# Kernel tuning notes

Hardware: AMD Instinct MI355X
Metric: run time of the kernel (lower is better)

The kernel has to match this reference:

```python
import jax, jax.numpy as jnp
import numpy as np

N, E = 100000, 800000
H, C = 4, 32
HC = H * C


def setup_inputs() -> dict:
    key = jax.random.key(0)
    ks = jax.random.split(key, 32)

    def lin(k, fi, fo):
        return jax.random.normal(k, (fi, fo), jnp.float32) / np.sqrt(fi)

    inp = {
        "x": jax.random.normal(ks[0], (N, 2), jnp.float32),
        "edge_index": jax.random.randint(ks[1], (2, E), 0, N, jnp.int64),
        "edge_attr": jax.random.normal(ks[2], (E, 1), jnp.float32),
        # layer 0 (in=2)
        "Wq0": lin(ks[3], 2, HC), "bq0": jnp.zeros((HC,), jnp.float32),
        "Wk0": lin(ks[4], 2, HC), "bk0": jnp.zeros((HC,), jnp.float32),
        "Wv0": lin(ks[5], 2, HC), "bv0": jnp.zeros((HC,), jnp.float32),
        "We0": lin(ks[6], 1, HC),
        "Ws0": lin(ks[7], 2, HC), "bs0": jnp.zeros((HC,), jnp.float32),
        # layer 1 (in=HC)
        "Wq1": lin(ks[8], HC, HC), "bq1": jnp.zeros((HC,), jnp.float32),
        "Wk1": lin(ks[9], HC, HC), "bk1": jnp.zeros((HC,), jnp.float32),
        "Wv1": lin(ks[10], HC, HC), "bv1": jnp.zeros((HC,), jnp.float32),
        "We1": lin(ks[11], 1, HC),
        "Ws1": lin(ks[12], HC, HC), "bs1": jnp.zeros((HC,), jnp.float32),
        # classifier
        "Wc1": lin(ks[13], HC, 128), "bc1": jnp.zeros((128,), jnp.float32),
        "Wc2": lin(ks[14], 128, 64), "bc2": jnp.zeros((64,), jnp.float32),
        "Wc3": lin(ks[15], 64, 1), "bc3": jnp.zeros((1,), jnp.float32),
    }
    return inp


def _tconv(x, src, dst, edge_attr, Wq, bq, Wk, bk, Wv, bv, We, Ws, bs):
    # PyG TransformerConv (concat=True, root_weight=True, beta=False)
    n = x.shape[0]
    q = (x @ Wq + bq).reshape(n, H, C)
    k = (x @ Wk + bk).reshape(n, H, C)
    v = (x @ Wv + bv).reshape(n, H, C)
    e = (edge_attr @ We).reshape(-1, H, C)            # [E,H,C]
    k_j = k[src] + e
    v_j = v[src] + e
    alpha = jnp.einsum("ehc,ehc->eh", q[dst], k_j) / np.sqrt(C)  # [E,H]
    m = jax.ops.segment_max(alpha, dst, num_segments=n)          # [n,H]
    m = jnp.where(jnp.isfinite(m), m, 0.0)            # nodes with no in-edges
    ex = jnp.exp(alpha - m[dst])
    denom = jax.ops.segment_sum(ex, dst, num_segments=n)
    w = ex / (denom[dst] + 1e-16)                      # per-edge softmax weight
    out = jax.ops.segment_sum(v_j * w[:, :, None], dst, num_segments=n)
    return out.reshape(n, HC) + x @ Ws + bs


def reference(x, edge_index, edge_attr,
              Wq0, bq0, Wk0, bk0, Wv0, bv0, We0, Ws0, bs0,
              Wq1, bq1, Wk1, bk1, Wv1, bv1, We1, Ws1, bs1,
              Wc1, bc1, Wc2, bc2, Wc3, bc3):
    src, dst = edge_index[0], edge_index[1]
    h = jax.nn.relu(_tconv(x, src, dst, edge_attr, Wq0, bq0, Wk0, bk0, Wv0, bv0, We0, Ws0, bs0))
    h = jax.nn.relu(_tconv(h, src, dst, edge_attr, Wq1, bq1, Wk1, bk1, Wv1, bv1, We1, Ws1, bs1))
    # classifier (dropout inactive in eval)
    h = jax.nn.relu(h @ Wc1 + bc1)
    h = jax.nn.relu(h @ Wc2 + bc2)
    return h @ Wc3 + bc3
```

## Files before the change

### kernel.cpp

```cpp
#include <hip/hip_runtime.h>
#include <hip/hip_bf16.h>
#include <cstdio>
#include <cstdint>


typedef short s16x8 __attribute__((ext_vector_type(8)));
typedef float f32x4 __attribute__((ext_vector_type(4)));

static inline int cdiv(int a, int b) { return (a + b - 1) / b; }

#define EXP2F(x) __builtin_amdgcn_exp2f(x)
#define LOG2E 1.4426950408889634f
#define RSC 0.17677669529663687f

__device__ __forceinline__ float bflo(unsigned u) {
    union { unsigned i; float f; } x; x.i = u << 16; return x.f;
}
__device__ __forceinline__ float bfhi(unsigned u) {
    union { unsigned i; float f; } x; x.i = u & 0xffff0000u; return x.f;
}
__device__ __forceinline__ unsigned short f2b(float f) {
    __hip_bfloat16 h = __float2bfloat16(f);
    return *reinterpret_cast<unsigned short*>(&h);
}
__device__ __forceinline__ unsigned packbf(float lo, float hi) {
    return (unsigned)f2b(lo) | ((unsigned)f2b(hi) << 16);
}


__global__ __launch_bounds__(256) void hist_kernel(const int* __restrict__ dst, int E,
                                                   int* __restrict__ counts) {
    int e = blockIdx.x * 256 + threadIdx.x;
    if (e < E) atomicAdd(&counts[dst[e]], 1);
}

__global__ __launch_bounds__(256) void scan_sums(const int* __restrict__ counts, int n,
                                                 int* __restrict__ bsums) {
    __shared__ int red[256];
    int base = blockIdx.x * 2048 + threadIdx.x * 8;
    int s = 0;
#pragma unroll
    for (int j = 0; j < 8; ++j) {
        int i = base + j;
        if (i < n) s += counts[i];
    }
    red[threadIdx.x] = s;
    __syncthreads();
    for (int off = 128; off > 0; off >>= 1) {
        if (threadIdx.x < off) red[threadIdx.x] += red[threadIdx.x + off];
        __syncthreads();
    }
    if (threadIdx.x == 0) bsums[blockIdx.x] = red[0];
}

__global__ void scan_mid(int* bsums, int nb, int* offsets, int n) {
    if (blockIdx.x == 0 && threadIdx.x == 0) {
        int run = 0;
        for (int i = 0; i < nb; ++i) { int t = bsums[i]; bsums[i] = run; run += t; }
        offsets[n] = run;
    }
}

__global__ __launch_bounds__(256) void scan_out(const int* __restrict__ counts, int n,
                                                const int* __restrict__ bsums,
                                                int* __restrict__ offsets) {
    __shared__ int tsum[256];
    int base = blockIdx.x * 2048 + threadIdx.x * 8;
    int v[8];
    int s = 0;
#pragma unroll
    for (int j = 0; j < 8; ++j) {
        int i = base + j;
        v[j] = (i < n) ? counts[i] : 0;
        s += v[j];
    }
    tsum[threadIdx.x] = s;
    __syncthreads();
    for (int off = 1; off < 256; off <<= 1) {
        int x = (threadIdx.x >= (unsigned)off) ? tsum[threadIdx.x - off] : 0;
        __syncthreads();
        tsum[threadIdx.x] += x;
        __syncthreads();
    }
    int excl = tsum[threadIdx.x] - s + bsums[blockIdx.x];
#pragma unroll
    for (int j = 0; j < 8; ++j) {
        int i = base + j;
        if (i < n) { offsets[i] = excl; excl += v[j]; }
    }
}

__global__ __launch_bounds__(256) void scatter_kernel(const int* __restrict__ src,
                                                      const int* __restrict__ dst,
                                                      const float* __restrict__ ea, int E,
                                                      const int* __restrict__ offsets,
                                                      int* __restrict__ counts,
                                                      int* __restrict__ csr_off,
                                                      float* __restrict__ csr_ea) {
    int e = blockIdx.x * 256 + threadIdx.x;
    if (e >= E) return;
    int d = dst[e];
    int r = atomicSub(&counts[d], 1);
    int p = offsets[d] + r - 1;
    csr_off[p] = src[e] << 9;
    csr_ea[p] = ea[e];
}


__global__ __launch_bounds__(256) void pack_w_kernel(
    const float* __restrict__ Wq1, const float* __restrict__ Wk1,
    const float* __restrict__ Wv1, const float* __restrict__ Ws1,
    const float* __restrict__ Wc1, const float* __restrict__ Wc2,
    unsigned short* __restrict__ wpk,
    const float* __restrict__ Wq0, const float* __restrict__ bq0,
    const float* __restrict__ Wk0, const float* __restrict__ bk0,
    const float* __restrict__ We0, float* __restrict__ gcoef) {
    if (blockIdx.x == 352) {
        int t = threadIdx.x;
        if (t < 48) {
            int h = t / 12, r = t % 12, i = r >> 2, j = r & 3;
            const float* A = (i == 0) ? Wq0 : (i == 1) ? (Wq0 + 128) : bq0;
            const float* B = (j == 0) ? Wk0 : (j == 1) ? (Wk0 + 128) : (j == 2) ? We0 : bk0;
            float s = 0.f;
            for (int c = 0; c < 32; ++c) s += A[h * 32 + c] * B[h * 32 + c];
            gcoef[h * 12 + i * 4 + j] = s * (RSC * LOG2E);
        }
        return;
    }
    int idx = blockIdx.x * 256 + threadIdx.x;
    int local, COLS;
    const float* W;
    if (idx < 81920) {
        int m = idx >> 14;
        local = idx & 16383;
        COLS = 128;
        W = (m == 0) ? Wq1 : (m == 1) ? Wk1 : (m == 2) ? Wv1 : (m == 3) ? Ws1 : Wc1;
    } else {
        local = idx - 81920;
        COLS = 64;
        W = Wc2;
    }
    int CT = COLS >> 4;
    int j = local & 7, lane = (local >> 3) & 63, t = local >> 9;
    int ct = t % CT, kc = t / CT;
    int k = kc * 32 + ((lane >> 4) << 3) + j;
    int nn = (ct << 4) + (lane & 15);
    wpk[idx] = f2b(W[k * COLS + nn]);
}


__global__ __launch_bounds__(256) void agg0_kernel(
    const float* __restrict__ x, const float* __restrict__ gcoef,
    float4* __restrict__ agg4,
    const int* __restrict__ offsets, const int* __restrict__ csr_off,
    const float* __restrict__ csr_ea, int n_nodes) {
    int tid = blockIdx.x * 256 + threadIdx.x;
    int n = tid >> 2, h = tid & 3;
    if (n >= n_nodes) return;
    float2 xn = ((const float2*)x)[n];
    const float4* G4 = (const float4*)gcoef;
    float4 g0 = G4[h * 3 + 0], g1 = G4[h * 3 + 1], g2 = G4[h * 3 + 2];
    float c0 = fmaf(xn.y, g1.x, fmaf(xn.x, g0.x, g2.x));
    float c1 = fmaf(xn.y, g1.y, fmaf(xn.x, g0.y, g2.y));
    float c2 = fmaf(xn.y, g1.z, fmaf(xn.x, g0.z, g2.z));
    float c3 = fmaf(xn.y, g1.w, fmaf(xn.x, g0.w, g2.w));
    int beg = offsets[n], end = offsets[n + 1];
    float d = 0.f, X0 = 0.f, X1 = 0.f, EA = 0.f;
    for (int j = beg; j < end; ++j) {
        int off = csr_off[j];
        float e = csr_ea[j];
        float2 xs = *(const float2*)((const char*)x + (off >> 6));
        float al = fmaf(c0, xs.x, fmaf(c1, xs.y, fmaf(c2, e, c3)));
        float w = EXP2F(fminf(al, 72.f));
        d += w;
        X0 = fmaf(w, xs.x, X0);
        X1 = fmaf(w, xs.y, X1);
        EA = fmaf(w, e, EA);
    }
    agg4[(size_t)n * 4 + h] = make_float4(X0, X1, EA, d);
}


__global__ __launch_bounds__(256) void expand0_kernel(
    const float* __restrict__ x, const float4* __restrict__ agg4,
    const float* __restrict__ Wv, const float* __restrict__ bv,
    const float* __restrict__ We, const float* __restrict__ Ws,
    const float* __restrict__ bs, uint2* __restrict__ H0, int n_nodes) {
    int gid = blockIdx.x * 256 + threadIdx.x;
    int n = gid >> 5, g = gid & 31;
    if (n >= n_nodes) return;
    int h = g >> 3;
    float4 ag = agg4[(size_t)n * 4 + h];
    float inv = 1.f / (ag.w + 1e-16f);
    float2 xn = ((const float2*)x)[n];
    float4 wv0 = ((const float4*)Wv)[g], wv1 = ((const float4*)(Wv + 128))[g];
    float4 we = ((const float4*)We)[g], bv4 = ((const float4*)bv)[g];
    float4 ws0 = ((const float4*)Ws)[g], ws1 = ((const float4*)(Ws + 128))[g];
    float4 bs4 = ((const float4*)bs)[g];
    float o0 = fmaf(wv0.x, ag.x, fmaf(wv1.x, ag.y, fmaf(we.x, ag.z, bv4.x * ag.w))) * inv
             + fmaf(xn.x, ws0.x, fmaf(xn.y, ws1.x, bs4.x));
    float o1 = fmaf(wv0.y, ag.x, fmaf(wv1.y, ag.y, fmaf(we.y, ag.z, bv4.y * ag.w))) * inv
             + fmaf(xn.x, ws0.y, fmaf(xn.y, ws1.y, bs4.y));
    float o2 = fmaf(wv0.z, ag.x, fmaf(wv1.z, ag.y, fmaf(we.z, ag.z, bv4.z * ag.w))) * inv
             + fmaf(xn.x, ws0.z, fmaf(xn.y, ws1.z, bs4.z));
    float o3 = fmaf(wv0.w, ag.x, fmaf(wv1.w, ag.y, fmaf(we.w, ag.z, bv4.w * ag.w))) * inv
             + fmaf(xn.x, ws0.w, fmaf(xn.y, ws1.w, bs4.w));
    uint2 o;
    o.x = packbf(fmaxf(o0, 0.f), fmaxf(o1, 0.f));
    o.y = packbf(fmaxf(o2, 0.f), fmaxf(o3, 0.f));
    H0[(size_t)n * 32 + g] = o;
}


__global__ __launch_bounds__(64) void agg1_kernel(
    const uint2* __restrict__ Q2, const unsigned short* __restrict__ KV,
    const float* __restrict__ We, const uint2* __restrict__ S2,
    uint2* __restrict__ Hout, const int* __restrict__ offsets,
    const int* __restrict__ csr_off, const float* __restrict__ csr_ea,
    int n_nodes) {
    int lane = threadIdx.x & 63;
    int h = lane & 31, half = lane >> 5;
    int n = blockIdx.x;
    if (n >= n_nodes) return;
    size_t rb = (size_t)n * 32;
    const float sc = RSC * LOG2E;
    uint2 qp = Q2[rb + h];
    float q0 = bflo(qp.x) * sc, q1 = bfhi(qp.x) * sc;
    float q2 = bflo(qp.y) * sc, q3 = bfhi(qp.y) * sc;
    float4 we4 = ((const float4*)We)[h];
    float qwe = fmaf(q3, we4.w, fmaf(q2, we4.z, fmaf(q1, we4.y, q0 * we4.x)));
    qwe += __shfl_xor(qwe, 1);
    qwe += __shfl_xor(qwe, 2);
    qwe += __shfl_xor(qwe, 4);
    int beg = __builtin_amdgcn_readfirstlane(offsets[n]);
    int end = __builtin_amdgcn_readfirstlane(offsets[n + 1]);
    float dA = 0.f, a0A = 0.f, a1A = 0.f, a2A = 0.f, a3A = 0.f, eA = 0.f;
    float dB = 0.f, a0B = 0.f, a1B = 0.f, a2B = 0.f, a3B = 0.f, eB = 0.f;
    int lane_b = h << 3;
    for (int j = beg + half; j < end; j += 4) {
        int jB = j + 2;
        bool vB = jB < end;
        int jmB = vB ? jB : j;
        int offA = csr_off[j], offB = csr_off[jmB];
        float eaA = csr_ea[j], eaB = csr_ea[jmB];
        const char* kvA = (const char*)KV + (size_t)(unsigned)offA + lane_b;
        const char* kvB = (const char*)KV + (size_t)(unsigned)offB + lane_b;
        uint2 kA = *(const uint2*)kvA;
        uint2 vA = *(const uint2*)(kvA + 256);
        uint2 kB = *(const uint2*)kvB;
        uint2 vB2 = *(const uint2*)(kvB + 256);
        {
            float p = fmaf(q3, bfhi(kA.y), fmaf(q2, bflo(kA.y),
                      fmaf(q1, bfhi(kA.x), q0 * bflo(kA.x))));
            p += __shfl_xor(p, 1);
            p += __shfl_xor(p, 2);
            p += __shfl_xor(p, 4);
            float al = fminf(fmaf(eaA, qwe, p), 72.f);
            float w = EXP2F(al);
            dA += w;
            a0A = fmaf(w, bflo(vA.x), a0A);
            a1A = fmaf(w, bfhi(vA.x), a1A);
            a2A = fmaf(w, bflo(vA.y), a2A);
            a3A = fmaf(w, bfhi(vA.y), a3A);
            eA = fmaf(w, eaA, eA);
        }
        {
            float p = fmaf(q3, bfhi(kB.y), fmaf(q2, bflo(kB.y),
                      fmaf(q1, bfhi(kB.x), q0 * bflo(kB.x))));
            p += __shfl_xor(p, 1);
            p += __shfl_xor(p, 2);
            p += __shfl_xor(p, 4);
            float al = fmaf(eaB, qwe, p);
            al = vB ? al : -3.0e38f;
            float w = EXP2F(fminf(al, 72.f));
            dB += w;
            a0B = fmaf(w, bflo(vB2.x), a0B);
            a1B = fmaf(w, bfhi(vB2.x), a1B);
            a2B = fmaf(w, bflo(vB2.y), a2B);
            a3B = fmaf(w, bfhi(vB2.y), a3B);
            eB = fmaf(w, eaB, eB);
        }
    }
    float d = dA + dB;
    float a0 = a0A + a0B, a1 = a1A + a1B, a2 = a2A + a2B, a3 = a3A + a3B;
    float ea = eA + eB;
    d += __shfl_xor(d, 32);
    a0 += __shfl_xor(a0, 32);
    a1 += __shfl_xor(a1, 32);
    a2 += __shfl_xor(a2, 32);
    a3 += __shfl_xor(a3, 32);
    ea += __shfl_xor(ea, 32);
    if (half == 0) {
        float inv = 1.f / (d + 1e-16f);
        uint2 sp = S2[rb + h];
        uint2 o;
        o.x = packbf(fmaxf(fmaf(a0 + we4.x * ea, inv, bflo(sp.x)), 0.f),
                     fmaxf(fmaf(a1 + we4.y * ea, inv, bfhi(sp.x)), 0.f));
        o.y = packbf(fmaxf(fmaf(a2 + we4.z * ea, inv, bflo(sp.y)), 0.f),
                     fmaxf(fmaf(a3 + we4.w * ea, inv, bfhi(sp.y)), 0.f));
        Hout[rb + h] = o;
    }
}


__global__ __launch_bounds__(256, 2) void gemm4_kernel(
    const unsigned short* __restrict__ Hb, int n_nodes,
    const unsigned short* __restrict__ wpk,
    const float* __restrict__ B0, unsigned short* __restrict__ O0, int ld0,
    const float* __restrict__ B1, unsigned short* __restrict__ O1, int ld1,
    const float* __restrict__ B2, unsigned short* __restrict__ O2, int ld2,
    const float* __restrict__ B3, unsigned short* __restrict__ O3, int ld3) {
    __shared__ unsigned short wbuf[16384];
    __shared__ char tbuf[128 * 272];
    int tid = threadIdx.x;
    int wid = tid >> 6, lane = tid & 63;
    int lr = lane & 15, lk = lane >> 4;
    int nblk = blockIdx.x * 128;

    s16x8 b[2][4];
#pragma unroll
    for (int nt = 0; nt < 2; ++nt) {
        int row = min(nblk + wid * 32 + nt * 16 + lr, n_nodes - 1);
        const s16x8* hp = (const s16x8*)(Hb + (size_t)row * 128);
#pragma unroll
        for (int kc = 0; kc < 4; ++kc) b[nt][kc] = hp[kc * 4 + lk];
    }
    const float* Bm[4] = {B0, B1, B2, B3};
    unsigned short* Om[4] = {O0, O1, O2, O3};
    int ldm[4] = {ld0, ld1, ld2, ld3};

#pragma unroll
    for (int i = 0; i < 8; ++i) {
        int c = i * 256 + tid;
        ((uint4*)wbuf)[c] = ((const uint4*)wpk)[c];
    }
#pragma unroll
    for (int mm = 0; mm < 4; ++mm) {
        __syncthreads();
        f32x4 acc[2][8];
#pragma unroll
        for (int nt = 0; nt < 2; ++nt)
#pragma unroll
            for (int ct = 0; ct < 8; ++ct) acc[nt][ct] = (f32x4){0.f, 0.f, 0.f, 0.f};
#pragma unroll
        for (int kc = 0; kc < 4; ++kc) {
#pragma unroll
            for (int ct = 0; ct < 8; ++ct) {
                s16x8 a = ((const s16x8*)wbuf)[(kc * 8 + ct) * 64 + lane];
                acc[0][ct] = __builtin_amdgcn_mfma_f32_16x16x32_bf16(a, b[0][kc], acc[0][ct], 0, 0, 0);
                acc[1][ct] = __builtin_amdgcn_mfma_f32_16x16x32_bf16(a, b[1][kc], acc[1][ct], 0, 0, 0);
            }
        }
        const float* Bp = Bm[mm];
#pragma unroll
        for (int ct = 0; ct < 8; ++ct) {
            float4 bb = *(const float4*)(Bp + ct * 16 + lk * 4);
#pragma unroll
            for (int nt = 0; nt < 2; ++nt) {
                int rnode = wid * 32 + nt * 16 + lr;
                uint2 o;
                o.x = packbf(acc[nt][ct][0] + bb.x, acc[nt][ct][1] + bb.y);
                o.y = packbf(acc[nt][ct][2] + bb.z, acc[nt][ct][3] + bb.w);
                *(uint2*)(tbuf + rnode * 272 + ct * 32 + lk * 8) = o;
            }
        }
        __syncthreads();
        unsigned short* Op = Om[mm];
        int ld = ldm[mm];
#pragma unroll
        for (int i = 0; i < 8; ++i) {
            int chunk = i * 256 + tid;
            int nd = chunk >> 4, c16 = chunk & 15;
            int ng = nblk + nd;
            uint4 v = *(const uint4*)(tbuf + nd * 272 + c16 * 16);
            if (ng < n_nodes) *(uint4*)(Op + (size_t)ng * ld + c16 * 8) = v;
        }
        if (mm < 3) {
            const uint4* ws = (const uint4*)(wpk + (mm + 1) * 16384);
#pragma unroll
            for (int i = 0; i < 8; ++i) {
                int c = i * 256 + tid;
                ((uint4*)wbuf)[c] = ws[c];
            }
        }
    }
}


__global__ __launch_bounds__(256) void classifier_kernel(
    const unsigned short* __restrict__ H1b, int n_nodes,
    const unsigned short* __restrict__ wc1p, const float* __restrict__ bc1,
    const unsigned short* __restrict__ wc2p, const float* __restrict__ bc2,
    const float* __restrict__ Wc3, const float* __restrict__ bc3,
    float* __restrict__ out) {
    __shared__ char lds_raw[4 * 16 * 272];
    int wid = threadIdx.x >> 6, lane = threadIdx.x & 63;
    int lr = lane & 15, lk = lane >> 4;
    int nb = blockIdx.x * 64 + wid * 16;
    char* tile = lds_raw + wid * 16 * 272;

    s16x8 b[4];
    {
        int row = min(nb + lr, n_nodes - 1);
        const s16x8* hp = (const s16x8*)(H1b + (size_t)row * 128);
#pragma unroll
        for (int kc = 0; kc < 4; ++kc) b[kc] = hp[kc * 4 + lk];
    }
    f32x4 acc[8];
#pragma unroll
    for (int ct = 0; ct < 8; ++ct) acc[ct] = (f32x4){0.f, 0.f, 0.f, 0.f};
#pragma unroll
    for (int kc = 0; kc < 4; ++kc)
#pragma unroll
        for (int ct = 0; ct < 8; ++ct) {
            s16x8 a = ((const s16x8*)wc1p)[(kc * 8 + ct) * 64 + lane];
            acc[ct] = __builtin_amdgcn_mfma_f32_16x16x32_bf16(a, b[kc], acc[ct], 0, 0, 0);
        }
#pragma unroll
    for (int ct = 0; ct < 8; ++ct) {
        float4 bb = *(const float4*)(bc1 + ct * 16 + lk * 4);
        uint2 o;
        o.x = packbf(fmaxf(acc[ct][0] + bb.x, 0.f), fmaxf(acc[ct][1] + bb.y, 0.f));
        o.y = packbf(fmaxf(acc[ct][2] + bb.z, 0.f), fmaxf(acc[ct][3] + bb.w, 0.f));
        *(uint2*)(tile + lr * 272 + ct * 32 + lk * 8) = o;
    }
    __syncthreads();
    s16x8 b2[4];
#pragma unroll
    for (int kc = 0; kc < 4; ++kc)
        b2[kc] = *(const s16x8*)(tile + lr * 272 + kc * 64 + lk * 16);
    f32x4 acc2[4];
#pragma unroll
    for (int ct = 0; ct < 4; ++ct) acc2[ct] = (f32x4){0.f, 0.f, 0.f, 0.f};
#pragma unroll
    for (int kc = 0; kc < 4; ++kc)
#pragma unroll
        for (int ct = 0; ct < 4; ++ct) {
            s16x8 a = ((const s16x8*)wc2p)[(kc * 4 + ct) * 64 + lane];
            acc2[ct] = __builtin_amdgcn_mfma_f32_16x16x32_bf16(a, b2[kc], acc2[ct], 0, 0, 0);
        }
    float part = 0.f;
#pragma unroll
    for (int ct = 0; ct < 4; ++ct) {
        int ch0 = ct * 16 + lk * 4;
        float4 bb = *(const float4*)(bc2 + ch0);
        float4 w3 = *(const float4*)(Wc3 + ch0);
        part += fmaxf(acc2[ct][0] + bb.x, 0.f) * w3.x;
        part += fmaxf(acc2[ct][1] + bb.y, 0.f) * w3.y;
        part += fmaxf(acc2[ct][2] + bb.z, 0.f) * w3.z;
        part += fmaxf(acc2[ct][3] + bb.w, 0.f) * w3.w;
    }
    part += __shfl_xor(part, 16);
    part += __shfl_xor(part, 32);
    if (lk == 0) {
        int node = nb + lr;
        if (node < n_nodes) out[node] = part + bc3[0];
    }
}


extern "C" void kernel_launch(void* const* d_in, const int* in_sizes, int n_in,
                              void* d_out, int out_size, void* d_ws, size_t ws_size,
                              hipStream_t stream) {
    const float* x = (const float*)d_in[0];
    const int* ei = (const int*)d_in[1];
    const float* ea = (const float*)d_in[2];
    const float *Wq0 = (const float*)d_in[3], *bq0 = (const float*)d_in[4];
    const float *Wk0 = (const float*)d_in[5], *bk0 = (const float*)d_in[6];
    const float *Wv0 = (const float*)d_in[7], *bv0 = (const float*)d_in[8];
    const float* We0 = (const float*)d_in[9];
    const float *Ws0 = (const float*)d_in[10], *bs0 = (const float*)d_in[11];
    const float *Wq1 = (const float*)d_in[12], *bq1 = (const float*)d_in[13];
    const float *Wk1 = (const float*)d_in[14], *bk1 = (const float*)d_in[15];
    const float *Wv1 = (const float*)d_in[16], *bv1 = (const float*)d_in[17];
    const float* We1 = (const float*)d_in[18];
    const float *Ws1 = (const float*)d_in[19], *bs1 = (const float*)d_in[20];
    const float *Wc1 = (const float*)d_in[21], *bc1 = (const float*)d_in[22];
    const float *Wc2 = (const float*)d_in[23], *bc2 = (const float*)d_in[24];
    const float *Wc3 = (const float*)d_in[25], *bc3 = (const float*)d_in[26];

    const int N = in_sizes[0] / 2;
    const int E = in_sizes[2];
    const int* src = ei;
    const int* dst = ei + E;

    size_t NM = (size_t)N * 128;
    float4* agg4 = (float4*)d_ws;
    float* gcoef = (float*)(agg4 + (size_t)N * 4);
    unsigned short* H0b = (unsigned short*)(gcoef + 64);
    unsigned short* Qb = H0b + NM;
    unsigned short* KV = Qb + NM;
    unsigned short* S1b = KV + 2 * NM;
    unsigned short* wpk = S1b + NM;
    int* counts = (int*)(wpk + 90112);
    int* offsets = counts + N;
    int* bsums = offsets + N + 1;
    int* csr_off = bsums + 256;
    float* csr_ea = (float*)(csr_off + E);
    size_t need = (size_t)((char*)(csr_ea + E) - (char*)d_ws);
    if (need > ws_size) {
        fprintf(stderr, "kernel_launch: ws too small (need %zu, have %zu)\n", need, ws_size);
        return;
    }

    const int NB_SCAN = cdiv(N, 2048);

    hipMemsetAsync(counts, 0, (size_t)N * 4, stream);
    hist_kernel<<<cdiv(E, 256), 256, 0, stream>>>(dst, E, counts);
    scan_sums<<<NB_SCAN, 256, 0, stream>>>(counts, N, bsums);
    scan_mid<<<1, 64, 0, stream>>>(bsums, NB_SCAN, offsets, N);
    scan_out<<<NB_SCAN, 256, 0, stream>>>(counts, N, bsums, offsets);
    scatter_kernel<<<cdiv(E, 256), 256, 0, stream>>>(src, dst, ea, E, offsets, counts,
                                                     csr_off, csr_ea);
    pack_w_kernel<<<353, 256, 0, stream>>>(Wq1, Wk1, Wv1, Ws1, Wc1, Wc2, wpk,
                                           Wq0, bq0, Wk0, bk0, We0, gcoef);

    agg0_kernel<<<cdiv(N * 4, 256), 256, 0, stream>>>(
        x, gcoef, agg4, offsets, csr_off, csr_ea, N);
    expand0_kernel<<<cdiv(N * 32, 256), 256, 0, stream>>>(
        x, agg4, Wv0, bv0, We0, Ws0, bs0, (uint2*)H0b, N);

    gemm4_kernel<<<cdiv(N, 128), 256, 0, stream>>>(
        H0b, N, wpk,
        bq1, Qb, 128,
        bk1, KV, 256,
        bv1, KV + 128, 256,
        bs1, S1b, 128);
    agg1_kernel<<<N, 64, 0, stream>>>(
        (const uint2*)Qb, KV, We1, (const uint2*)S1b, (uint2*)S1b,
        offsets, csr_off, csr_ea, N);

    classifier_kernel<<<cdiv(N, 64), 256, 0, stream>>>(
        S1b, N, wpk + 65536, bc1, wpk + 81920, bc2, Wc3, bc3, (float*)d_out);
}
```

Before: 353.1 us.

## Interleave CSR offset/attr, widen agg1 to 16-byte loads, stage classifier weights in LDS

Result: slower. 360.3 us (+2.1%).

```diff
diff --git a/kernel.cpp b/kernel.cpp
--- a/kernel.cpp
+++ b/kernel.cpp
@@ -95,15 +95,13 @@
                                                       const float* __restrict__ ea, int E,
                                                       const int* __restrict__ offsets,
                                                       int* __restrict__ counts,
-                                                      int* __restrict__ csr_off,
-                                                      float* __restrict__ csr_ea) {
+                                                      int2* __restrict__ csr) {
     int e = blockIdx.x * 256 + threadIdx.x;
     if (e >= E) return;
     int d = dst[e];
     int r = atomicSub(&counts[d], 1);
     int p = offsets[d] + r - 1;
-    csr_off[p] = src[e] << 9;
-    csr_ea[p] = ea[e];
+    csr[p] = make_int2(src[e] << 9, __float_as_int(ea[e]));
 }
 
 
@@ -152,8 +150,7 @@
 __global__ __launch_bounds__(256) void agg0_kernel(
     const float* __restrict__ x, const float* __restrict__ gcoef,
     float4* __restrict__ agg4,
-    const int* __restrict__ offsets, const int* __restrict__ csr_off,
-    const float* __restrict__ csr_ea, int n_nodes) {
+    const int* __restrict__ offsets, const int2* __restrict__ csr, int n_nodes) {
     int tid = blockIdx.x * 256 + threadIdx.x;
     int n = tid >> 2, h = tid & 3;
     if (n >= n_nodes) return;
@@ -167,9 +164,9 @@
     int beg = offsets[n], end = offsets[n + 1];
     float d = 0.f, X0 = 0.f, X1 = 0.f, EA = 0.f;
     for (int j = beg; j < end; ++j) {
-        int off = csr_off[j];
-        float e = csr_ea[j];
-        float2 xs = *(const float2*)((const char*)x + (off >> 6));
+        int2 ce = csr[j];
+        float e = __int_as_float(ce.y);
+        float2 xs = *(const float2*)((const char*)x + (((unsigned)ce.x) >> 6));
         float al = fmaf(c0, xs.x, fmaf(c1, xs.y, fmaf(c2, e, c3)));
         float w = EXP2F(fminf(al, 72.f));
         d += w;
@@ -213,91 +210,107 @@
 
 
 __global__ __launch_bounds__(64) void agg1_kernel(
-    const uint2* __restrict__ Q2, const unsigned short* __restrict__ KV,
-    const float* __restrict__ We, const uint2* __restrict__ S2,
-    uint2* __restrict__ Hout, const int* __restrict__ offsets,
-    const int* __restrict__ csr_off, const float* __restrict__ csr_ea,
-    int n_nodes) {
+    const uint4* __restrict__ Q4, const unsigned short* __restrict__ KV,
+    const float* __restrict__ We, const uint4* __restrict__ S4,
+    uint4* __restrict__ Hout, const int* __restrict__ offsets,
+    const int2* __restrict__ csr, int n_nodes) {
     int lane = threadIdx.x & 63;
-    int h = lane & 31, half = lane >> 5;
+    int h = lane & 15, g = lane >> 4;
     int n = blockIdx.x;
     if (n >= n_nodes) return;
-    size_t rb = (size_t)n * 32;
+    size_t rb = (size_t)n * 16;
     const float sc = RSC * LOG2E;
-    uint2 qp = Q2[rb + h];
+    uint4 qp = Q4[rb + h];
     float q0 = bflo(qp.x) * sc, q1 = bfhi(qp.x) * sc;
     float q2 = bflo(qp.y) * sc, q3 = bfhi(qp.y) * sc;
-    float4 we4 = ((const float4*)We)[h];
-    float qwe = fmaf(q3, we4.w, fmaf(q2, we4.z, fmaf(q1, we4.y, q0 * we4.x)));
+    float q4 = bflo(qp.z) * sc, q5 = bfhi(qp.z) * sc;
+    float q6 = bflo(qp.w) * sc, q7 = bfhi(qp.w) * sc;
+    float4 wea = ((const float4*)We)[2 * h], web = ((const float4*)We)[2 * h + 1];
+    float qwe = fmaf(q7, web.w, fmaf(q6, web.z, fmaf(q5, web.y, fmaf(q4, web.x,
+                fmaf(q3, wea.w, fmaf(q2, wea.z, fmaf(q1, wea.y, q0 * wea.x)))))));
     qwe += __shfl_xor(qwe, 1);
     qwe += __shfl_xor(qwe, 2);
-    qwe += __shfl_xor(qwe, 4);
     int beg = __builtin_amdgcn_readfirstlane(offsets[n]);
     int end = __builtin_amdgcn_readfirstlane(offsets[n + 1]);
-    float dA = 0.f, a0A = 0.f, a1A = 0.f, a2A = 0.f, a3A = 0.f, eA = 0.f;
-    float dB = 0.f, a0B = 0.f, a1B = 0.f, a2B = 0.f, a3B = 0.f, eB = 0.f;
-    int lane_b = h << 3;
-    for (int j = beg + half; j < end; j += 4) {
-        int jB = j + 2;
-        bool vB = jB < end;
-        int jmB = vB ? jB : j;
-        int offA = csr_off[j], offB = csr_off[jmB];
-        float eaA = csr_ea[j], eaB = csr_ea[jmB];
-        const char* kvA = (const char*)KV + (size_t)(unsigned)offA + lane_b;
-        const char* kvB = (const char*)KV + (size_t)(unsigned)offB + lane_b;
-        uint2 kA = *(const uint2*)kvA;
-        uint2 vA = *(const uint2*)(kvA + 256);
-        uint2 kB = *(const uint2*)kvB;
-        uint2 vB2 = *(const uint2*)(kvB + 256);
+    float dA = 0.f, eA = 0.f, dB = 0.f, eB = 0.f;
+    float aA0 = 0.f, aA1 = 0.f, aA2 = 0.f, aA3 = 0.f;
+    float aA4 = 0.f, aA5 = 0.f, aA6 = 0.f, aA7 = 0.f;
+    float aB0 = 0.f, aB1 = 0.f, aB2 = 0.f, aB3 = 0.f;
+    float aB4 = 0.f, aB5 = 0.f, aB6 = 0.f, aB7 = 0.f;
+    int hb = h << 4;
+    for (int t = beg; t < end; t += 8) {
+        int jA = t + g, jB = jA + 4;
+        bool vA = jA < end, vB = jB < end;
+        int2 ceA = csr[vA ? jA : beg];
+        int2 ceB = csr[vB ? jB : beg];
+        float eaA = __int_as_float(ceA.y), eaB = __int_as_float(ceB.y);
+        const char* kvA = (const char*)KV + (size_t)(unsigned)ceA.x + hb;
+        const char* kvB = (const char*)KV + (size_t)(unsigned)ceB.x + hb;
+        uint4 kA = *(const uint4*)kvA;
+        uint4 vA4 = *(const uint4*)(kvA + 256);
+        uint4 kB = *(const uint4*)kvB;
+        uint4 vB4 = *(const uint4*)(kvB + 256);
         {
-            float p = fmaf(q3, bfhi(kA.y), fmaf(q2, bflo(kA.y),
-                      fmaf(q1, bfhi(kA.x), q0 * bflo(kA.x))));
+            float p = fmaf(q7, bfhi(kA.w), fmaf(q6, bflo(kA.w), fmaf(q5, bfhi(kA.z),
+                      fmaf(q4, bflo(kA.z), fmaf(q3, bfhi(kA.y), fmaf(q2, bflo(kA.y),
+                      fmaf(q1, bfhi(kA.x), q0 * bflo(kA.x))))))));
             p += __shfl_xor(p, 1);
             p += __shfl_xor(p, 2);
-            p += __shfl_xor(p, 4);
             float al = fminf(fmaf(eaA, qwe, p), 72.f);
+            al = vA ? al : -3.0e38f;
             float w = EXP2F(al);
             dA += w;
-            a0A = fmaf(w, bflo(vA.x), a0A);
-            a1A = fmaf(w, bfhi(vA.x), a1A);
-            a2A = fmaf(w, bflo(vA.y), a2A);
-            a3A = fmaf(w, bfhi(vA.y), a3A);
             eA = fmaf(w, eaA, eA);
+            aA0 = fmaf(w, bflo(vA4.x), aA0); aA1 = fmaf(w, bfhi(vA4.x), aA1);
+            aA2 = fmaf(w, bflo(vA4.y), aA2); aA3 = fmaf(w, bfhi(vA4.y), aA3);
+            aA4 = fmaf(w, bflo(vA4.z), aA4); aA5 = fmaf(w, bfhi(vA4.z), aA5);
+            aA6 = fmaf(w, bflo(vA4.w), aA6); aA7 = fmaf(w, bfhi(vA4.w), aA7);
         }
         {
-            float p = fmaf(q3, bfhi(kB.y), fmaf(q2, bflo(kB.y),
-                      fmaf(q1, bfhi(kB.x), q0 * bflo(kB.x))));
+            float p = fmaf(q7, bfhi(kB.w), fmaf(q6, bflo(kB.w), fmaf(q5, bfhi(kB.z),
+                      fmaf(q4, bflo(kB.z), fmaf(q3, bfhi(kB.y), fmaf(q2, bflo(kB.y),
+                      fmaf(q1, bfhi(kB.x), q0 * bflo(kB.x))))))));
             p += __shfl_xor(p, 1);
             p += __shfl_xor(p, 2);
-            p += __shfl_xor(p, 4);
-            float al = fmaf(eaB, qwe, p);
+            float al = fminf(fmaf(eaB, qwe, p), 72.f);
             al = vB ? al : -3.0e38f;
-            float w = EXP2F(fminf(al, 72.f));
+            float w = EXP2F(al);
             dB += w;
-            a0B = fmaf(w, bflo(vB2.x), a0B);
-            a1B = fmaf(w, bfhi(vB2.x), a1B);
-            a2B = fmaf(w, bflo(vB2.y), a2B);
-            a3B = fmaf(w, bfhi(vB2.y), a3B);
             eB = fmaf(w, eaB, eB);
-        }
-    }
-    float d = dA + dB;
-    float a0 = a0A + a0B, a1 = a1A + a1B, a2 = a2A + a2B, a3 = a3A + a3B;
-    float ea = eA + eB;
-    d += __shfl_xor(d, 32);
-    a0 += __shfl_xor(a0, 32);
-    a1 += __shfl_xor(a1, 32);
-    a2 += __shfl_xor(a2, 32);
-    a3 += __shfl_xor(a3, 32);
-    ea += __shfl_xor(ea, 32);
-    if (half == 0) {
+            aB0 = fmaf(w, bflo(vB4.x), aB0); aB1 = fmaf(w, bfhi(vB4.x), aB1);
+            aB2 = fmaf(w, bflo(vB4.y), aB2); aB3 = fmaf(w, bfhi(vB4.y), aB3);
+            aB4 = fmaf(w, bflo(vB4.z), aB4); aB5 = fmaf(w, bfhi(vB4.z), aB5);
+            aB6 = fmaf(w, bflo(vB4.w), aB6); aB7 = fmaf(w, bfhi(vB4.w), aB7);
+        }
+    }
+    float d = dA + dB, ea = eA + eB;
+    float a0 = aA0 + aB0, a1 = aA1 + aB1, a2 = aA2 + aB2, a3 = aA3 + aB3;
+    float a4 = aA4 + aB4, a5 = aA5 + aB5, a6 = aA6 + aB6, a7 = aA7 + aB7;
+#pragma unroll
+    for (int mk = 16; mk < 64; mk <<= 1) {
+        d += __shfl_xor(d, mk);
+        ea += __shfl_xor(ea, mk);
+        a0 += __shfl_xor(a0, mk); a1 += __shfl_xor(a1, mk);
+        a2 += __shfl_xor(a2, mk); a3 += __shfl_xor(a3, mk);
+        a4 += __shfl_xor(a4, mk); a5 += __shfl_xor(a5, mk);
+        a6 += __shfl_xor(a6, mk); a7 += __shfl_xor(a7, mk);
+    }
+    if (g == 0) {
         float inv = 1.f / (d + 1e-16f);
-        uint2 sp = S2[rb + h];
-        uint2 o;
-        o.x = packbf(fmaxf(fmaf(a0 + we4.x * ea, inv, bflo(sp.x)), 0.f),
-                     fmaxf(fmaf(a1 + we4.y * ea, inv, bfhi(sp.x)), 0.f));
-        o.y = packbf(fmaxf(fmaf(a2 + we4.z * ea, inv, bflo(sp.y)), 0.f),
-                     fmaxf(fmaf(a3 + we4.w * ea, inv, bfhi(sp.y)), 0.f));
+        uint4 sp = S4[rb + h];
+        float o0 = fmaf(fmaf(wea.x, ea, a0), inv, bflo(sp.x));
+        float o1 = fmaf(fmaf(wea.y, ea, a1), inv, bfhi(sp.x));
+        float o2 = fmaf(fmaf(wea.z, ea, a2), inv, bflo(sp.y));
+        float o3 = fmaf(fmaf(wea.w, ea, a3), inv, bfhi(sp.y));
+        float o4 = fmaf(fmaf(web.x, ea, a4), inv, bflo(sp.z));
+        float o5 = fmaf(fmaf(web.y, ea, a5), inv, bfhi(sp.z));
+        float o6 = fmaf(fmaf(web.z, ea, a6), inv, bflo(sp.w));
+        float o7 = fmaf(fmaf(web.w, ea, a7), inv, bfhi(sp.w));
+        uint4 o;
+        o.x = packbf(fmaxf(o0, 0.f), fmaxf(o1, 0.f));
+        o.y = packbf(fmaxf(o2, 0.f), fmaxf(o3, 0.f));
+        o.z = packbf(fmaxf(o4, 0.f), fmaxf(o5, 0.f));
+        o.w = packbf(fmaxf(o6, 0.f), fmaxf(o7, 0.f));
         Hout[rb + h] = o;
     }
 }
@@ -310,8 +323,8 @@
     const float* __restrict__ B1, unsigned short* __restrict__ O1, int ld1,
     const float* __restrict__ B2, unsigned short* __restrict__ O2, int ld2,
     const float* __restrict__ B3, unsigned short* __restrict__ O3, int ld3) {
-    __shared__ unsigned short wbuf[16384];
-    __shared__ char tbuf[128 * 272];
+    __shared__ __align__(16) unsigned short wbuf[16384];
+    __shared__ __align__(16) char tbuf[128 * 272];
     int tid = threadIdx.x;
     int wid = tid >> 6, lane = tid & 63;
     int lr = lane & 15, lk = lane >> 4;
@@ -387,17 +400,27 @@
 }
 
 
-__global__ __launch_bounds__(256) void classifier_kernel(
+__global__ __launch_bounds__(256, 2) void classifier_kernel(
     const unsigned short* __restrict__ H1b, int n_nodes,
     const unsigned short* __restrict__ wc1p, const float* __restrict__ bc1,
     const unsigned short* __restrict__ wc2p, const float* __restrict__ bc2,
     const float* __restrict__ Wc3, const float* __restrict__ bc3,
     float* __restrict__ out) {
-    __shared__ char lds_raw[4 * 16 * 272];
-    int wid = threadIdx.x >> 6, lane = threadIdx.x & 63;
+    __shared__ __align__(16) unsigned short w1s[16384];
+    __shared__ __align__(16) unsigned short w2s[8192];
+    __shared__ __align__(16) char lds_raw[4 * 16 * 272];
+    int tid = threadIdx.x;
+    int wid = tid >> 6, lane = tid & 63;
     int lr = lane & 15, lk = lane >> 4;
     int nb = blockIdx.x * 64 + wid * 16;
     char* tile = lds_raw + wid * 16 * 272;
+
+#pragma unroll
+    for (int i = 0; i < 8; ++i)
+        ((uint4*)w1s)[i * 256 + tid] = ((const uint4*)wc1p)[i * 256 + tid];
+#pragma unroll
+    for (int i = 0; i < 4; ++i)
+        ((uint4*)w2s)[i * 256 + tid] = ((const uint4*)wc2p)[i * 256 + tid];
 
     s16x8 b[4];
     {
@@ -406,6 +429,7 @@
 #pragma unroll
         for (int kc = 0; kc < 4; ++kc) b[kc] = hp[kc * 4 + lk];
     }
+    __syncthreads();
     f32x4 acc[8];
 #pragma unroll
     for (int ct = 0; ct < 8; ++ct) acc[ct] = (f32x4){0.f, 0.f, 0.f, 0.f};
@@ -413,7 +437,7 @@
     for (int kc = 0; kc < 4; ++kc)
 #pragma unroll
         for (int ct = 0; ct < 8; ++ct) {
-            s16x8 a = ((const s16x8*)wc1p)[(kc * 8 + ct) * 64 + lane];
+            s16x8 a = ((const s16x8*)w1s)[(kc * 8 + ct) * 64 + lane];
             acc[ct] = __builtin_amdgcn_mfma_f32_16x16x32_bf16(a, b[kc], acc[ct], 0, 0, 0);
         }
 #pragma unroll
@@ -436,7 +460,7 @@
     for (int kc = 0; kc < 4; ++kc)
 #pragma unroll
         for (int ct = 0; ct < 4; ++ct) {
-            s16x8 a = ((const s16x8*)wc2p)[(kc * 4 + ct) * 64 + lane];
+            s16x8 a = ((const s16x8*)w2s)[(kc * 4 + ct) * 64 + lane];
             acc2[ct] = __builtin_amdgcn_mfma_f32_16x16x32_bf16(a, b2[kc], acc2[ct], 0, 0, 0);
         }
     float part = 0.f;
@@ -495,9 +519,8 @@
     int* counts = (int*)(wpk + 90112);
     int* offsets = counts + N;
     int* bsums = offsets + N + 1;
-    int* csr_off = bsums + 256;
-    float* csr_ea = (float*)(csr_off + E);
-    size_t need = (size_t)((char*)(csr_ea + E) - (char*)d_ws);
+    int2* csr = (int2*)(bsums + 256);
+    size_t need = (size_t)((char*)(csr + E) - (char*)d_ws);
     if (need > ws_size) {
         fprintf(stderr, "kernel_launch: ws too small (need %zu, have %zu)\n", need, ws_size);
         return;
@@ -510,13 +533,12 @@
     scan_sums<<<NB_SCAN, 256, 0, stream>>>(counts, N, bsums);
     scan_mid<<<1, 64, 0, stream>>>(bsums, NB_SCAN, offsets, N);
     scan_out<<<NB_SCAN, 256, 0, stream>>>(counts, N, bsums, offsets);
-    scatter_kernel<<<cdiv(E, 256), 256, 0, stream>>>(src, dst, ea, E, offsets, counts,
-                                                     csr_off, csr_ea);
+    scatter_kernel<<<cdiv(E, 256), 256, 0, stream>>>(src, dst, ea, E, offsets, counts, csr);
     pack_w_kernel<<<353, 256, 0, stream>>>(Wq1, Wk1, Wv1, Ws1, Wc1, Wc2, wpk,
                                            Wq0, bq0, Wk0, bk0, We0, gcoef);
 
     agg0_kernel<<<cdiv(N * 4, 256), 256, 0, stream>>>(
-        x, gcoef, agg4, offsets, csr_off, csr_ea, N);
+        x, gcoef, agg4, offsets, csr, N);
     expand0_kernel<<<cdiv(N * 32, 256), 256, 0, stream>>>(
         x, agg4, Wv0, bv0, We0, Ws0, bs0, (uint2*)H0b, N);
 
@@ -527,8 +549,8 @@
         bv1, KV + 128, 256,
         bs1, S1b, 128);
     agg1_kernel<<<N, 64, 0, stream>>>(
-        (const uint2*)Qb, KV, We1, (const uint2*)S1b, (uint2*)S1b,
-        offsets, csr_off, csr_ea, N);
+        (const uint4*)Qb, KV, We1, (const uint4*)S1b, (uint4*)S1b,
+        offsets, csr, N);
 
     classifier_kernel<<<cdiv(N, 64), 256, 0, stream>>>(
         S1b, N, wpk + 65536, bc1, wpk + 81920, bc2, Wc3, bc3, (float*)d_out);
```
